# Kernel optimization log

Hardware: AMD Instinct MI355X
Metric: run time of the kernel (lower is better)

Reference implementation:

```python
import jax, jax.numpy as jnp
from jax import lax
import numpy as np
from jax.scipy.special import logsumexp

B, T, K = 64, 4096, 32

def setup_inputs() -> dict:
    key = jax.random.key(0)
    k1, k2, k3 = jax.random.split(key, 3)
    return {
        "emission_logp": jax.random.normal(k1, (B, T, K), dtype=jnp.float32),
        "log_pi": jax.random.normal(k2, (K,), dtype=jnp.float32),
        "log_A": jax.random.normal(k3, (K, K), dtype=jnp.float32),
    }

def reference(emission_logp, log_pi, log_A):
    b, t, k = emission_logp.shape
    lp = jax.nn.log_softmax(log_pi)            # [K]
    lA = jax.nn.log_softmax(log_A, axis=1)     # [K,K]
    em = jnp.swapaxes(emission_logp, 0, 1)     # [T,B,K] time-major for scan

    # forward recursion: alpha_t = logsumexp_i(alpha_{t-1,i} + A_{i,j}) + em_t
    a0 = lp[None, :] + em[0]                   # [B,K]
    def fstep(a_prev, e_t):
        a_new = logsumexp(a_prev[:, :, None] + lA[None, :, :], axis=1) + e_t
        return a_new, a_new
    _, alphas = lax.scan(fstep, a0, em[1:])
    alpha = jnp.concatenate([a0[None], alphas], axis=0)  # [T,B,K]

    # backward recursion: beta_t = logsumexp_j(beta_{t+1,j} + A_{i,j} + em_{t+1,j})
    bT = jnp.zeros((b, k), dtype=emission_logp.dtype)
    def bstep(b_next, e_next):
        b_new = logsumexp(b_next[:, None, :] + lA[None, :, :] + e_next[:, None, :], axis=2)
        return b_new, b_new
    _, betas = lax.scan(bstep, bT, em[1:], reverse=True)
    beta = jnp.concatenate([betas, bT[None]], axis=0)    # [T,B,K]

    log_gamma = alpha + beta
    log_gamma = log_gamma - logsumexp(log_gamma, axis=-1, keepdims=True)
    return jnp.swapaxes(log_gamma, 0, 1)       # [B,T,K]
```

## Files before the change

kernel.cpp:

```cpp
#include <hip/hip_runtime.h>

#define B_ 64
#define T_ 4096
#define K_ 32
#define C_ 512
#define L_ 8
#define W_ 28
#define PFD 4
#define NS (W_ + L_)

typedef float f32x16 __attribute__((ext_vector_type(16)));
typedef float f32x4v __attribute__((ext_vector_type(4)));
typedef short s16x8 __attribute__((ext_vector_type(8)));

union W4 { unsigned u[4]; short s[8]; s16x8 v; };

__device__ __forceinline__ unsigned cvt_pk_bf16(float lo, float hi) {
  unsigned r;
  asm("v_cvt_pk_bf16_f32 %0, %1, %2" : "=v"(r) : "v"(lo), "v"(hi));
  return r;
}
__device__ __forceinline__ short f2bf(float x) {
  unsigned u = __float_as_uint(x);
  return (short)((u + 0x7FFFu + ((u >> 16) & 1u)) >> 16);
}
__device__ __forceinline__ float wmax32(float v) {
#pragma unroll
  for (int k = 16; k >= 1; k >>= 1) v = fmaxf(v, __shfl_xor(v, k, 32));
  return v;
}
__device__ __forceinline__ float wsum32(float v) {
#pragma unroll
  for (int k = 16; k >= 1; k >>= 1) v += __shfl_xor(v, k, 32);
  return v;
}

__global__ __launch_bounds__(256) void pet_kernel(const float* __restrict__ em,
                                                  const float* __restrict__ log_pi,
                                                  const float* __restrict__ log_A,
                                                  float* __restrict__ eA,
                                                  float* __restrict__ lp,
                                                  unsigned* __restrict__ peP) {
  const int bid = (int)blockIdx.x;
  const int tid = (int)threadIdx.x;
  if (bid >= T_) {
    const int i0 = tid >> 5, j = tid & 31;
#pragma unroll
    for (int rr = 0; rr < 4; ++rr) {
      int i = i0 + 8 * rr;
      float a = log_A[i * K_ + j];
      float m = wmax32(a);
      float e = __expf(a - m);
      float S = wsum32(e);
      eA[i * K_ + j] = e / S;
    }
    if (i0 == 0) {
      float v = log_pi[j];
      float m2 = wmax32(v);
      float ee = __expf(v - m2);
      float SS = wsum32(ee);
      lp[j] = v - m2 - __logf(SS);
    }
    return;
  }
  const int t = ((bid & 7) << 9) + (bid >> 3);
  __shared__ float tile[K_][B_];
  const int b = tid >> 2, kq = tid & 3;
  const float* p = em + (size_t)b * (T_ * K_) + (size_t)t * K_ + kq * 8;
  f32x4v v0 = *(const f32x4v*)p;
  f32x4v v1 = *(const f32x4v*)(p + 4);
#pragma unroll
  for (int q = 0; q < 4; ++q) tile[kq * 8 + q][b] = __expf(v0[q]);
#pragma unroll
  for (int q = 0; q < 4; ++q) tile[kq * 8 + 4 + q][b] = __expf(v1[q]);
  __syncthreads();
  unsigned* ob = peP + (size_t)t * 1024;
#pragma unroll
  for (int rr = 0; rr < 4; ++rr) {
    int Wd = tid + 256 * rr;
    int col = Wd & 63, wq = (Wd >> 6) & 7, hh = Wd >> 9;
    int s0 = 2 * (wq & 1) + 8 * (wq >> 1) + 4 * hh;
    ob[Wd] = cvt_pk_bf16(tile[s0][col], tile[s0 + 1][col]);
  }
}

__global__ __launch_bounds__(128) void hmm2_kernel(const unsigned* __restrict__ peP,
                                                   const float* __restrict__ eA,
                                                   const float* __restrict__ lp,
                                                   float* __restrict__ out) {
  __shared__ __align__(16) unsigned aw[L_ * 512];
  __shared__ __align__(16) unsigned bw[L_ * 512];
  const int bid = (int)blockIdx.x;
  const int c = ((bid & 7) << 6) + ((bid >> 3) & 63);
  const int g = bid >> 9;
  const int tid = (int)threadIdx.x;
  const int wv = tid >> 6;
  const int l = tid & 63;
  const int h = l >> 5;
  const int m = l & 31;
  const int t0 = c * L_;
  const unsigned* pB = peP + (h << 9) + (g << 5) + m;

  f32x16 zk;
#pragma unroll
  for (int r = 0; r < 16; ++r) zk[r] = 0.0f;

  W4 A1u, A2u, B1u, B2u;
#pragma unroll
  for (int r = 0; r < 8; ++r) {
    const int k1 = (r & 3) + 8 * (r >> 2) + 4 * h;
    const int k2 = k1 + 16;
    float a1 = (wv == 0) ? eA[k1 * K_ + m] : eA[m * K_ + k1];
    float a2 = (wv == 0) ? eA[k2 * K_ + m] : eA[m * K_ + k2];
    A1u.s[r] = f2bf(a1);
    A2u.s[r] = f2bf(a2);
  }
#pragma unroll
  for (int q = 0; q < 4; ++q) { B1u.u[q] = 0x3F803F80u; B2u.u[q] = 0x3F803F80u; }

  unsigned ring[PFD][8];
  if (wv == 0) {
#pragma unroll
    for (int u = 0; u < PFD; ++u) {
      int tt = t0 - W_ + u; if (tt < 0) tt = 0;
      const unsigned* pp = pB + (size_t)tt * 1024;
#pragma unroll
      for (int w = 0; w < 8; ++w) ring[u][w] = pp[w * 64];
    }
  } else {
#pragma unroll
    for (int u = 0; u < PFD; ++u) {
      int tt = t0 + L_ - 1 + W_ - u; if (tt > T_ - 1) tt = T_ - 1;
      const unsigned* pp = pB + (size_t)tt * 1024;
#pragma unroll
      for (int w = 0; w < 8; ++w) ring[u][w] = pp[w * 64];
    }
  }

#define FSTEP(S)                                                               \
  {                                                                            \
    const int t = t0 + ((S) - W_);                                             \
    unsigned rg[8];                                                            \
    _Pragma("unroll") for (int w = 0; w < 8; ++w) rg[w] = ring[(S) & 3][w];    \
    f32x16 acc = __builtin_amdgcn_mfma_f32_32x32x16_bf16(A1u.v, B1u.v, zk, 0, 0, 0); \
    acc = __builtin_amdgcn_mfma_f32_32x32x16_bf16(A2u.v, B2u.v, acc, 0, 0, 0); \
    if (t == 0) {             \
      _Pragma("unroll") for (int r = 0; r < 16; ++r)                           \
        acc[r] = __expf(lp[(r & 3) + 8 * (r >> 2) + 4 * h]);                   \
    }                                                                          \
    float al[16];                                                              \
    _Pragma("unroll") for (int w = 0; w < 8; ++w) {                            \
      al[2 * w]     = acc[2 * w]     * __uint_as_float(rg[w] << 16);           \
      al[2 * w + 1] = acc[2 * w + 1] * __uint_as_float(rg[w] & 0xFFFF0000u);   \
    }                                                                          \
    { int tn = t + PFD; if (tn < 0) tn = 0; if (tn > T_ - 1) tn = T_ - 1;      \
      const unsigned* pp = pB + (size_t)tn * 1024;                             \
      _Pragma("unroll") for (int w = 0; w < 8; ++w) ring[(S) & 3][w] = pp[w * 64]; } \
    if (((S) & 7) == 7) {                                                      \
      float a0 = __shfl(al[0], m, 64);                                         \
      float rs = __builtin_amdgcn_rcpf(a0);                                    \
      _Pragma("unroll") for (int r = 0; r < 16; ++r) al[r] *= rs;              \
    }                                                                          \
    W4 nB1, nB2;                                                               \
    _Pragma("unroll") for (int q = 0; q < 4; ++q) {                            \
      nB1.u[q] = cvt_pk_bf16(al[2 * q], al[2 * q + 1]);                        \
      nB2.u[q] = cvt_pk_bf16(al[8 + 2 * q], al[8 + 2 * q + 1]);                \
    }                                                                          \
    if ((S) >= W_) {                                                           \
      unsigned* bp = &aw[(((S) - W_) << 9) + h * 32 + m];                      \
      _Pragma("unroll") for (int q = 0; q < 4; ++q) {                          \
        bp[q * 64] = nB1.u[q];                                                 \
        bp[(4 + q) * 64] = nB2.u[q];                                           \
      }                                                                        \
    }                                                                          \
    B1u = nB1; B2u = nB2;                                                      \
  }

#define BSTEP(S)                                                               \
  {                                                                            \
    const int t = t0 + (L_ - 1 + W_ - (S));                                    \
    unsigned rg[8];                                                            \
    _Pragma("unroll") for (int w = 0; w < 8; ++w) rg[w] = ring[(S) & 3][w];    \
    f32x16 acc = __builtin_amdgcn_mfma_f32_32x32x16_bf16(A1u.v, B1u.v, zk, 0, 0, 0); \
    acc = __builtin_amdgcn_mfma_f32_32x32x16_bf16(A2u.v, B2u.v, acc, 0, 0, 0); \
    if (t == T_ - 1) {                         \
      _Pragma("unroll") for (int r = 0; r < 16; ++r) acc[r] = 1.0f;            \
    }                                                                          \
    if ((S) >= W_) {                                                           \
      W4 s1, s2;                                                               \
      _Pragma("unroll") for (int q = 0; q < 4; ++q) {                          \
        s1.u[q] = cvt_pk_bf16(acc[2 * q], acc[2 * q + 1]);                     \
        s2.u[q] = cvt_pk_bf16(acc[8 + 2 * q], acc[8 + 2 * q + 1]);             \
      }                                                                        \
      unsigned* bp = &bw[((L_ - 1 + W_ - (S)) << 9) + h * 32 + m];             \
      _Pragma("unroll") for (int q = 0; q < 4; ++q) {                          \
        bp[q * 64] = s1.u[q];                                                  \
        bp[(4 + q) * 64] = s2.u[q];                                            \
      }                                                                        \
    }                                                                          \
    float al[16];                                                              \
    _Pragma("unroll") for (int w = 0; w < 8; ++w) {                            \
      al[2 * w]     = acc[2 * w]     * __uint_as_float(rg[w] << 16);           \
      al[2 * w + 1] = acc[2 * w + 1] * __uint_as_float(rg[w] & 0xFFFF0000u);   \
    }                                                                          \
    { int tn = t - PFD; if (tn < 0) tn = 0; if (tn > T_ - 1) tn = T_ - 1;      \
      const unsigned* pp = pB + (size_t)tn * 1024;                             \
      _Pragma("unroll") for (int w = 0; w < 8; ++w) ring[(S) & 3][w] = pp[w * 64]; } \
    if (((S) & 7) == 7) {                                                      \
      float a0 = __shfl(al[0], m, 64);                                         \
      float rs = __builtin_amdgcn_rcpf(a0);                                    \
      _Pragma("unroll") for (int r = 0; r < 16; ++r) al[r] *= rs;              \
    }                                                                          \
    W4 nB1, nB2;                                                               \
    _Pragma("unroll") for (int q = 0; q < 4; ++q) {                            \
      nB1.u[q] = cvt_pk_bf16(al[2 * q], al[2 * q + 1]);                        \
      nB2.u[q] = cvt_pk_bf16(al[8 + 2 * q], al[8 + 2 * q + 1]);                \
    }                                                                          \
    B1u = nB1; B2u = nB2;                                                      \
  }

#define REP4F(B) FSTEP(B) FSTEP((B) + 1) FSTEP((B) + 2) FSTEP((B) + 3)
#define REP4B(B) BSTEP(B) BSTEP((B) + 1) BSTEP((B) + 2) BSTEP((B) + 3)

  if (wv == 0) {
    REP4F(0) REP4F(4) REP4F(8) REP4F(12) REP4F(16) REP4F(20) REP4F(24) REP4F(28) REP4F(32)
  } else {
    REP4B(0) REP4B(4) REP4B(8) REP4B(12) REP4B(16) REP4B(20) REP4B(24) REP4B(28) REP4B(32)
  }

  __syncthreads();

  {
#pragma unroll
    for (int rr = 0; rr < 4; ++rr) {
      const int row = (wv << 2) + rr;
      const unsigned* pa = aw + (row << 9) + (h << 5) + m;
      const unsigned* pb = bw + (row << 9) + (h << 5) + m;
      float gg[16];
      float s = 0.0f;
#pragma unroll
      for (int w = 0; w < 8; ++w) {
        unsigned ua = pa[w * 64], ub = pb[w * 64];
        gg[2 * w]     = __uint_as_float(ua << 16) * __uint_as_float(ub << 16);
        gg[2 * w + 1] = __uint_as_float(ua & 0xFFFF0000u) * __uint_as_float(ub & 0xFFFF0000u);
      }
#pragma unroll
      for (int r = 0; r < 16; ++r) s += gg[r];
      s += __shfl_xor(s, 32, 64);
      const float ls = __log2f(s);
      float* po = out + (size_t)((g << 5) + m) * (T_ * K_) + (size_t)(t0 + row) * K_;
#pragma unroll
      for (int w = 0; w < 8; ++w) {
        const int k0 = 2 * (w & 1) + 8 * (w >> 1) + 4 * h;
        float2 v;
        v.x = (__log2f(gg[2 * w]) - ls) * 0.6931471805599453f;
        v.y = (__log2f(gg[2 * w + 1]) - ls) * 0.6931471805599453f;
        *(float2*)(po + k0) = v;
      }
    }
  }
}

extern "C" void kernel_launch(void* const* d_in, const int* in_sizes, int n_in,
                              void* d_out, int out_size, void* d_ws, size_t ws_size,
                              hipStream_t stream) {
  const float* em = (const float*)d_in[0];
  const float* log_pi = (const float*)d_in[1];
  const float* log_A = (const float*)d_in[2];
  float* out = (float*)d_out;

  float* eA = (float*)d_ws;
  float* lp = eA + K_ * K_;
  unsigned* peP = (unsigned*)((char*)d_ws + 8192);

  pet_kernel<<<T_ + 1, 256, 0, stream>>>(em, log_pi, log_A, eA, lp, peP);
  hmm2_kernel<<<2 * C_, 128, 0, stream>>>(peP, eA, lp, out);
}
```

Before: 35.80 us.

## Stage emissions via async global-to-LDS loads and enlarge chunks with longer warmup

Reworks the HMM forward-backward chunk kernel so emission data for each step is fetched with global_load_lds directly into a double-buffered shared-memory staging area, replacing the per-thread register ring prefetch. The producer layout in pet_kernel changes so each lane reads 8 contiguous words with two 16-byte LDS reads. Chunk length grows from 8 to 32 steps and the warmup window from 28 to 32, giving 4x fewer blocks and less redundant warmup per output step. The trade-offs are fewer blocks and less parallelism, more shared memory per block, and explicit vmcnt waits and schedule barriers that limit how the compiler can interleave work.

Result: slower. 43.64 us (+21.9%).

```diff
diff --git a/kernel.cpp b/kernel.cpp
--- a/kernel.cpp
+++ b/kernel.cpp
@@ -3,11 +3,10 @@
 #define B_ 64
 #define T_ 4096
 #define K_ 32
-#define C_ 512
-#define L_ 8
-#define W_ 28
-#define PFD 4
-#define NS (W_ + L_)
+#define C_ 128
+#define L_ 32
+#define W_ 32
+#define NPH 32
 
 typedef float f32x16 __attribute__((ext_vector_type(16)));
 typedef float f32x4v __attribute__((ext_vector_type(4)));
@@ -33,6 +32,11 @@
 #pragma unroll
   for (int k = 16; k >= 1; k >>= 1) v += __shfl_xor(v, k, 32);
   return v;
+}
+__device__ __forceinline__ void gload_lds16(const unsigned* g, unsigned* s) {
+  __builtin_amdgcn_global_load_lds(
+      (const __attribute__((address_space(1))) unsigned*)g,
+      (__attribute__((address_space(3))) unsigned*)s, 16, 0, 0);
 }
 
 __global__ __launch_bounds__(256) void pet_kernel(const float* __restrict__ em,
@@ -64,7 +68,7 @@
     return;
   }
   const int t = ((bid & 7) << 9) + (bid >> 3);
-  __shared__ float tile[K_][B_];
+  __shared__ float tile[K_][65];
   const int b = tid >> 2, kq = tid & 3;
   const float* p = em + (size_t)b * (T_ * K_) + (size_t)t * K_ + kq * 8;
   f32x4v v0 = *(const f32x4v*)p;
@@ -77,10 +81,10 @@
   unsigned* ob = peP + (size_t)t * 1024;
 #pragma unroll
   for (int rr = 0; rr < 4; ++rr) {
-    int Wd = tid + 256 * rr;
-    int col = Wd & 63, wq = (Wd >> 6) & 7, hh = Wd >> 9;
-    int s0 = 2 * (wq & 1) + 8 * (wq >> 1) + 4 * hh;
-    ob[Wd] = cvt_pk_bf16(tile[s0][col], tile[s0 + 1][col]);
+    int W2 = tid + 256 * rr;
+    int bb = (W2 >> 3) & 63, w = W2 & 7, hh = W2 >> 9;
+    int s0 = 2 * (w & 1) + 8 * (w >> 1) + 4 * hh;
+    ob[W2] = cvt_pk_bf16(tile[s0][bb], tile[s0 + 1][bb]);
   }
 }
 
@@ -90,16 +94,19 @@
                                                    float* __restrict__ out) {
   __shared__ __align__(16) unsigned aw[L_ * 512];
   __shared__ __align__(16) unsigned bw[L_ * 512];
+  __shared__ __align__(16) unsigned peb[4096];
   const int bid = (int)blockIdx.x;
-  const int c = ((bid & 7) << 6) + ((bid >> 3) & 63);
-  const int g = bid >> 9;
+  const int c = ((bid & 7) << 4) + ((bid >> 3) & 15);
+  const int g = bid >> 7;
   const int tid = (int)threadIdx.x;
   const int wv = tid >> 6;
   const int l = tid & 63;
   const int h = l >> 5;
   const int m = l & 31;
   const int t0 = c * L_;
-  const unsigned* pB = peP + (h << 9) + (g << 5) + m;
+
+  unsigned* myped = &peb[wv * 2048];
+  const unsigned* psrc = peP + (g << 8) + (l << 2);
 
   f32x16 zk;
 #pragma unroll
@@ -118,44 +125,50 @@
 #pragma unroll
   for (int q = 0; q < 4; ++q) { B1u.u[q] = 0x3F803F80u; B2u.u[q] = 0x3F803F80u; }
 
-  unsigned ring[PFD][8];
-  if (wv == 0) {
-#pragma unroll
-    for (int u = 0; u < PFD; ++u) {
-      int tt = t0 - W_ + u; if (tt < 0) tt = 0;
-      const unsigned* pp = pB + (size_t)tt * 1024;
-#pragma unroll
-      for (int w = 0; w < 8; ++w) ring[u][w] = pp[w * 64];
-    }
+  float einit[16];
+  if (wv == 0 && c < 2) {
+#pragma unroll
+    for (int r = 0; r < 16; ++r) einit[r] = __expf(lp[(r & 3) + 8 * (r >> 2) + 4 * h]);
   } else {
 #pragma unroll
-    for (int u = 0; u < PFD; ++u) {
-      int tt = t0 + L_ - 1 + W_ - u; if (tt > T_ - 1) tt = T_ - 1;
-      const unsigned* pp = pB + (size_t)tt * 1024;
-#pragma unroll
-      for (int w = 0; w < 8; ++w) ring[u][w] = pp[w * 64];
-    }
+    for (int r = 0; r < 16; ++r) einit[r] = 0.0f;
+  }
+
+  asm volatile("s_waitcnt vmcnt(0)" ::: "memory");
+  __builtin_amdgcn_sched_barrier(0);
+
+#define ISSUE(PH, FWD)                                                         \
+  if ((PH) < NPH) {                                                            \
+    _Pragma("unroll") for (int s2 = 0; s2 < 2; ++s2) {                         \
+      int SS = (PH) * 2 + s2;                                                  \
+      int tt = (FWD) ? (t0 - W_ + SS) : (t0 + L_ - 1 + W_ - SS);               \
+      tt = tt < 0 ? 0 : (tt > T_ - 1 ? T_ - 1 : tt);                           \
+      const unsigned* sb = psrc + (size_t)tt * 1024;                           \
+      unsigned* db = myped + (((PH) & 1) << 10) + (s2 << 9);                   \
+      gload_lds16(sb, db);                                                     \
+      gload_lds16(sb + 512, db + 256);                                         \
+    }                                                                          \
   }
 
 #define FSTEP(S)                                                               \
   {                                                                            \
     const int t = t0 + ((S) - W_);                                             \
-    unsigned rg[8];                                                            \
-    _Pragma("unroll") for (int w = 0; w < 8; ++w) rg[w] = ring[(S) & 3][w];    \
+    const unsigned* rp = myped + ((((S) >> 1) & 1) << 10) + (((S) & 1) << 9) + h * 256 + m * 8; \
+    uint4 r0 = *(const uint4*)rp;                                              \
+    uint4 r1 = *(const uint4*)(rp + 4);                                        \
     f32x16 acc = __builtin_amdgcn_mfma_f32_32x32x16_bf16(A1u.v, B1u.v, zk, 0, 0, 0); \
     acc = __builtin_amdgcn_mfma_f32_32x32x16_bf16(A2u.v, B2u.v, acc, 0, 0, 0); \
     if (t == 0) {             \
-      _Pragma("unroll") for (int r = 0; r < 16; ++r)                           \
-        acc[r] = __expf(lp[(r & 3) + 8 * (r >> 2) + 4 * h]);                   \
-    }                                                                          \
+      _Pragma("unroll") for (int r = 0; r < 16; ++r) acc[r] = einit[r];        \
+    }                                                                          \
+    unsigned rg[8];                                                            \
+    rg[0] = r0.x; rg[1] = r0.y; rg[2] = r0.z; rg[3] = r0.w;                    \
+    rg[4] = r1.x; rg[5] = r1.y; rg[6] = r1.z; rg[7] = r1.w;                    \
     float al[16];                                                              \
     _Pragma("unroll") for (int w = 0; w < 8; ++w) {                            \
       al[2 * w]     = acc[2 * w]     * __uint_as_float(rg[w] << 16);           \
       al[2 * w + 1] = acc[2 * w + 1] * __uint_as_float(rg[w] & 0xFFFF0000u);   \
     }                                                                          \
-    { int tn = t + PFD; if (tn < 0) tn = 0; if (tn > T_ - 1) tn = T_ - 1;      \
-      const unsigned* pp = pB + (size_t)tn * 1024;                             \
-      _Pragma("unroll") for (int w = 0; w < 8; ++w) ring[(S) & 3][w] = pp[w * 64]; } \
     if (((S) & 7) == 7) {                                                      \
       float a0 = __shfl(al[0], m, 64);                                         \
       float rs = __builtin_amdgcn_rcpf(a0);                                    \
@@ -179,8 +192,9 @@
 #define BSTEP(S)                                                               \
   {                                                                            \
     const int t = t0 + (L_ - 1 + W_ - (S));                                    \
-    unsigned rg[8];                                                            \
-    _Pragma("unroll") for (int w = 0; w < 8; ++w) rg[w] = ring[(S) & 3][w];    \
+    const unsigned* rp = myped + ((((S) >> 1) & 1) << 10) + (((S) & 1) << 9) + h * 256 + m * 8; \
+    uint4 r0 = *(const uint4*)rp;                                              \
+    uint4 r1 = *(const uint4*)(rp + 4);                                        \
     f32x16 acc = __builtin_amdgcn_mfma_f32_32x32x16_bf16(A1u.v, B1u.v, zk, 0, 0, 0); \
     acc = __builtin_amdgcn_mfma_f32_32x32x16_bf16(A2u.v, B2u.v, acc, 0, 0, 0); \
     if (t == T_ - 1) {                         \
@@ -198,14 +212,14 @@
         bp[(4 + q) * 64] = s2.u[q];                                            \
       }                                                                        \
     }                                                                          \
+    unsigned rg[8];                                                            \
+    rg[0] = r0.x; rg[1] = r0.y; rg[2] = r0.z; rg[3] = r0.w;                    \
+    rg[4] = r1.x; rg[5] = r1.y; rg[6] = r1.z; rg[7] = r1.w;                    \
     float al[16];                                                              \
     _Pragma("unroll") for (int w = 0; w < 8; ++w) {                            \
       al[2 * w]     = acc[2 * w]     * __uint_as_float(rg[w] << 16);           \
       al[2 * w + 1] = acc[2 * w + 1] * __uint_as_float(rg[w] & 0xFFFF0000u);   \
     }                                                                          \
-    { int tn = t - PFD; if (tn < 0) tn = 0; if (tn > T_ - 1) tn = T_ - 1;      \
-      const unsigned* pp = pB + (size_t)tn * 1024;                             \
-      _Pragma("unroll") for (int w = 0; w < 8; ++w) ring[(S) & 3][w] = pp[w * 64]; } \
     if (((S) & 7) == 7) {                                                      \
       float a0 = __shfl(al[0], m, 64);                                         \
       float rs = __builtin_amdgcn_rcpf(a0);                                    \
@@ -219,21 +233,36 @@
     B1u = nB1; B2u = nB2;                                                      \
   }
 
-#define REP4F(B) FSTEP(B) FSTEP((B) + 1) FSTEP((B) + 2) FSTEP((B) + 3)
-#define REP4B(B) BSTEP(B) BSTEP((B) + 1) BSTEP((B) + 2) BSTEP((B) + 3)
+#define PHASE(PH, STEPM, FWD)                                                  \
+  {                                                                            \
+    asm volatile("s_waitcnt vmcnt(%0)" :: "i"((PH) < NPH - 1 ? 4 : 0) : "memory"); \
+    __builtin_amdgcn_sched_barrier(0);                                         \
+    STEPM((PH) * 2 + 0)                                                        \
+    STEPM((PH) * 2 + 1)                                                        \
+    __builtin_amdgcn_sched_barrier(0);                                         \
+    ISSUE((PH) + 2, FWD)                                                       \
+  }
+
+#define PH8(A, STEPM, FWD)                                                     \
+  PHASE((A) + 0, STEPM, FWD) PHASE((A) + 1, STEPM, FWD)                        \
+  PHASE((A) + 2, STEPM, FWD) PHASE((A) + 3, STEPM, FWD)                        \
+  PHASE((A) + 4, STEPM, FWD) PHASE((A) + 5, STEPM, FWD)                        \
+  PHASE((A) + 6, STEPM, FWD) PHASE((A) + 7, STEPM, FWD)
 
   if (wv == 0) {
-    REP4F(0) REP4F(4) REP4F(8) REP4F(12) REP4F(16) REP4F(20) REP4F(24) REP4F(28) REP4F(32)
+    ISSUE(0, 1) ISSUE(1, 1)
+    PH8(0, FSTEP, 1) PH8(8, FSTEP, 1) PH8(16, FSTEP, 1) PH8(24, FSTEP, 1)
   } else {
-    REP4B(0) REP4B(4) REP4B(8) REP4B(12) REP4B(16) REP4B(20) REP4B(24) REP4B(28) REP4B(32)
+    ISSUE(0, 0) ISSUE(1, 0)
+    PH8(0, BSTEP, 0) PH8(8, BSTEP, 0) PH8(16, BSTEP, 0) PH8(24, BSTEP, 0)
   }
 
   __syncthreads();
 
   {
 #pragma unroll
-    for (int rr = 0; rr < 4; ++rr) {
-      const int row = (wv << 2) + rr;
+    for (int rr = 0; rr < 16; ++rr) {
+      const int row = (wv << 4) + rr;
       const unsigned* pa = aw + (row << 9) + (h << 5) + m;
       const unsigned* pb = bw + (row << 9) + (h << 5) + m;
       float gg[16];
```
